# Performance work log

Measured on AMD Instinct MI355X. Metric: run time of the kernel, lower is better.

The kernel has to match this reference:

```python
import jax, jax.numpy as jnp
import numpy as np

EMBED_DIM = 1024
N_HEAD = 16
HEAD_DIM = EMBED_DIM // N_HEAD


def setup_inputs() -> dict:
    key = jax.random.key(0)
    k1, k2, k3 = jax.random.split(key, 3)
    B, S = 2, 2048
    x = jax.random.normal(k1, (B, S, EMBED_DIM), dtype=jnp.float32)
    # kaiming-style scale for the packed QKV projection and output projection
    w_qkv = jax.random.normal(k2, (3 * EMBED_DIM, EMBED_DIM), dtype=jnp.float32) * np.sqrt(2.0 / EMBED_DIM)
    w0 = jax.random.normal(k3, (EMBED_DIM, EMBED_DIM), dtype=jnp.float32) * np.sqrt(2.0 / EMBED_DIM)
    return {"x": x, "w_qkv": w_qkv, "w0": w0}


def reference(x, w_qkv, w0):
    B, S, E = x.shape
    # fused QKV projection (Linear with no bias): x @ w_qkv.T -> [B,S,3E]
    qkv = jnp.einsum('bse,fe->bsf', x, w_qkv)
    q, k, v = jnp.split(qkv, 3, axis=-1)
    # reshape to [B, H, S, D]
    def heads(t):
        return t.reshape(B, S, N_HEAD, HEAD_DIM).transpose(0, 2, 1, 3)
    q, k, v = heads(q), heads(k), heads(v)
    scale = 1.0 / np.sqrt(HEAD_DIM).astype(np.float32)
    scores = jnp.einsum('bhsd,bhtd->bhst', q, k) * scale  # [B,H,S,S]
    # causal additive bias: -inf above the diagonal (same math as the precomputed bias tensor)
    causal = jnp.tril(jnp.ones((S, S), dtype=bool))
    scores = jnp.where(causal, scores, -jnp.inf)
    probs = jax.nn.softmax(scores, axis=-1)
    e = jnp.einsum('bhst,bhtd->bhsd', probs, v)  # [B,H,S,D]
    e = e.transpose(0, 2, 1, 3).reshape(B, S, E)
    # output projection: E @ w0.T
    return jnp.einsum('bse,fe->bsf', e, w0)
```

## Files before the change

### kernel.cpp

```cpp
#include <hip/hip_runtime.h>


typedef unsigned short u16;
typedef short bf16x8 __attribute__((ext_vector_type(8)));
typedef float f32x4 __attribute__((ext_vector_type(4)));
typedef unsigned short u16x4 __attribute__((ext_vector_type(4)));

#define S_LEN 2048
#define EMB 1024
#define NH 16
#define HD 64
#define QKV_W 3072
#define BATCH 2
#define CSC 0.18033688f
#define PSTR 72

static __device__ __forceinline__ u16 f2bf(float f) {
    unsigned x = __float_as_uint(f);
    return (u16)((x + 0x7fffu + ((x >> 16) & 1u)) >> 16);
}

static __device__ __forceinline__ void gld_lds16(const u16* g, u16* l) {
    __builtin_amdgcn_global_load_lds(
        (const __attribute__((address_space(1))) void*)g,
        (__attribute__((address_space(3))) void*)l, 16, 0, 0);
}

#define XN4 (BATCH * S_LEN * EMB / 4)
#define WQ4 (QKV_W * EMB / 4)
#define W04 (EMB * EMB / 4)
__global__ __launch_bounds__(256) void cvt_all(const float* __restrict__ x,
                                               const float* __restrict__ wq,
                                               const float* __restrict__ w0,
                                               u16* __restrict__ xb,
                                               u16* __restrict__ wqb,
                                               u16* __restrict__ w0b) {
    int i = blockIdx.x * 256 + threadIdx.x;
    const float* src;
    u16* dst;
    int off;
    if (i < XN4) { src = x; dst = xb; off = i; }
    else if (i < XN4 + WQ4) { src = wq; dst = wqb; off = i - XN4; }
    else { src = w0; dst = w0b; off = i - XN4 - WQ4; }
    float4 v = ((const float4*)src)[off];
    u16x4 o;
    o[0] = f2bf(v.x); o[1] = f2bf(v.y); o[2] = f2bf(v.z); o[3] = f2bf(v.w);
    ((u16x4*)dst)[off] = o;
}

template <typename OutT, int BN>
__global__ __launch_bounds__(256) void gemm_bt(const u16* __restrict__ A,
                                               const u16* __restrict__ Bt,
                                               OutT* __restrict__ C,
                                               int M, int N, int K, int qcols) {
    constexpr int NF = BN / 32;
    __shared__ alignas(16) u16 As[128 * 32];
    __shared__ alignas(16) u16 Bs[BN * 32];
    const int tid = threadIdx.x;
    const int wave = tid >> 6, lane = tid & 63;
    const int quad = lane >> 4, lr = lane & 15;
    const int m0 = blockIdx.y * 128, n0 = blockIdx.x * BN;
    const int wm = (wave & 1) * 64, wn = (wave >> 1) * (BN / 2);
    const float sc = (n0 < qcols) ? CSC : 1.0f;

    f32x4 acc[4][NF] = {};

    for (int k0 = 0; k0 < K; k0 += 32) {
#pragma unroll
        for (int i = 0; i < 2; ++i) {
            int chunk = tid + i * 256;
            int row = chunk >> 2;
            int col8 = (chunk & 3) * 8;
            gld_lds16(&A[(size_t)(m0 + row) * K + k0 + col8], &As[row * 32 + col8]);
        }
#pragma unroll
        for (int i = 0; i < BN / 64; ++i) {
            int chunk = tid + i * 256;
            int row = chunk >> 2;
            int col8 = (chunk & 3) * 8;
            gld_lds16(&Bt[(size_t)(n0 + row) * K + k0 + col8], &Bs[row * 32 + col8]);
        }
        __syncthreads();
        bf16x8 af[4], bf[NF];
#pragma unroll
        for (int i = 0; i < 4; ++i)
            af[i] = *(const bf16x8*)&As[(wm + i * 16 + lr) * 32 + quad * 8];
#pragma unroll
        for (int i = 0; i < NF; ++i)
            bf[i] = *(const bf16x8*)&Bs[(wn + i * 16 + lr) * 32 + quad * 8];
#pragma unroll
        for (int mi = 0; mi < 4; ++mi)
#pragma unroll
            for (int ni = 0; ni < NF; ++ni)
                acc[mi][ni] = __builtin_amdgcn_mfma_f32_16x16x32_bf16(
                    af[mi], bf[ni], acc[mi][ni], 0, 0, 0);
        __syncthreads();
    }

#pragma unroll
    for (int mi = 0; mi < 4; ++mi) {
#pragma unroll
        for (int r = 0; r < 4; ++r) {
            int gr = m0 + wm + mi * 16 + quad * 4 + r;
#pragma unroll
            for (int ni = 0; ni < NF; ++ni) {
                int gc = n0 + wn + ni * 16 + lr;
                float v = acc[mi][ni][r] * sc;
                if constexpr (sizeof(OutT) == 2)
                    C[(size_t)gr * N + gc] = (OutT)f2bf(v);
                else
                    C[(size_t)gr * N + gc] = (OutT)v;
            }
        }
    }
}

__global__ __launch_bounds__(256) void transpose_v(const u16* __restrict__ qkv,
                                                   u16* __restrict__ vt) {
    __shared__ alignas(16) u16 t[64][72];
    const int s0 = blockIdx.x * 64;
    const int bh = blockIdx.y;
    const int b = bh >> 4, h = bh & 15;
#pragma unroll
    for (int i = 0; i < 2; ++i) {
        int chunk = threadIdx.x + i * 256;
        int row = chunk >> 3;
        int c8 = (chunk & 7) * 8;
        uint4 v = *(const uint4*)&qkv[(size_t)(b * S_LEN + s0 + row) * QKV_W +
                                      2 * EMB + h * HD + c8];
        const u16* p = (const u16*)&v;
#pragma unroll
        for (int jj = 0; jj < 8; ++jj) t[c8 + jj][row] = p[jj];
    }
    __syncthreads();
#pragma unroll
    for (int i = 0; i < 2; ++i) {
        int chunk = threadIdx.x + i * 256;
        int d = chunk >> 3;
        int c8 = (chunk & 7) * 8;
        uint4 v = *(const uint4*)&t[d][c8];
        *(uint4*)&vt[((size_t)bh * HD + d) * S_LEN + s0 + c8] = v;
    }
}

__global__ __launch_bounds__(512, 4) void attn(const u16* __restrict__ qkv,
                                               const u16* __restrict__ vt,
                                               u16* __restrict__ e) {
    const int tid = threadIdx.x;
    const int w = tid >> 6, lane = tid & 63;
    const int quad = lane >> 4, lr = lane & 15;
    const int pi = blockIdx.x;
    const int qtB = 31 - pi;
    const int bh = blockIdx.y, b = bh >> 4, h = bh & 15;
    const int myqt = (w < 4) ? pi : qtB;
    const int qbase = myqt * 64 + (w & 3) * 16;

    __shared__ alignas(16) u16 Ks[2 * 2 * 64 * 32];
    __shared__ alignas(16) u16 Vs[2 * 2 * 64 * 32];
    __shared__ alignas(16) u16 plds[8][16 * PSTR];
    u16* pw = plds[w];

    const u16* qkv_b = qkv + (size_t)b * S_LEN * QKV_W;
    const u16* qrow = qkv_b + (size_t)(qbase + lr) * QKV_W + h * HD + quad * 8;
    const bf16x8 qf0 = *(const bf16x8*)(qrow);
    const bf16x8 qf1 = *(const bf16x8*)(qrow + 32);

    const u16* kbase = qkv_b + EMB + h * HD;
    const u16* vbase = vt + (size_t)bh * HD * S_LEN;

    f32x4 o[4] = {};
    float lsum = 0.f;
    const int qg = qbase + lr;

    const int sr = (w & 3) * 16 + (lane >> 2);
    const int sc = (lane & 3) * 8;

    auto stage = [&](int j, int bb) {
        const int kv0 = j * 64;
        if (w < 4) {
            gld_lds16(kbase + (size_t)(kv0 + sr) * QKV_W + sc,
                      &Ks[bb * 4096 + sr * 32 + sc]);
            gld_lds16(kbase + (size_t)(kv0 + sr) * QKV_W + 32 + sc,
                      &Ks[bb * 4096 + 2048 + sr * 32 + sc]);
        } else {
            gld_lds16(vbase + (size_t)sr * S_LEN + kv0 + sc,
                      &Vs[bb * 4096 + sr * 32 + sc]);
            gld_lds16(vbase + (size_t)sr * S_LEN + kv0 + 32 + sc,
                      &Vs[bb * 4096 + 2048 + sr * 32 + sc]);
        }
    };

    stage(0, 0);
    for (int j = 0; j <= qtB; ++j) {
        const int bb = j & 1;
        __syncthreads();
        if (j < qtB) stage(j + 1, 1 - bb);
        if (j <= myqt) {
            const int kv0 = j * 64;
            const u16* ks = &Ks[bb * 4096];
            const u16* vs = &Vs[bb * 4096];
            f32x4 s[4];
#pragma unroll
            for (int nt = 0; nt < 4; ++nt) {
                bf16x8 k0 = *(const bf16x8*)&ks[(nt * 16 + lr) * 32 + quad * 8];
                bf16x8 k1 = *(const bf16x8*)&ks[2048 + (nt * 16 + lr) * 32 + quad * 8];
                f32x4 z = {};
                z = __builtin_amdgcn_mfma_f32_16x16x32_bf16(k0, qf0, z, 0, 0, 0);
                z = __builtin_amdgcn_mfma_f32_16x16x32_bf16(k1, qf1, z, 0, 0, 0);
                s[nt] = z;
            }
            const bool diag = (j == myqt);
            __builtin_amdgcn_wave_barrier();
#pragma unroll
            for (int nt = 0; nt < 4; ++nt) {
                float p[4];
#pragma unroll
                for (int r = 0; r < 4; ++r) {
                    float pv = exp2f(s[nt][r]);
                    if (diag) pv = (kv0 + nt * 16 + quad * 4 + r > qg) ? 0.f : pv;
                    p[r] = pv;
                }
                lsum += (p[0] + p[1]) + (p[2] + p[3]);
                uint2 pk;
                pk.x = __builtin_amdgcn_perm(__float_as_uint(p[1]),
                                             __float_as_uint(p[0]), 0x07060302u);
                pk.y = __builtin_amdgcn_perm(__float_as_uint(p[3]),
                                             __float_as_uint(p[2]), 0x07060302u);
                *(uint2*)&pw[lr * PSTR + nt * 16 + quad * 4] = pk;
            }
            __builtin_amdgcn_wave_barrier();
            const bf16x8 p0 = *(const bf16x8*)&pw[lr * PSTR + quad * 8];
            const bf16x8 p1 = *(const bf16x8*)&pw[lr * PSTR + 32 + quad * 8];
#pragma unroll
            for (int nt = 0; nt < 4; ++nt) {
                bf16x8 v0 = *(const bf16x8*)&vs[(nt * 16 + lr) * 32 + quad * 8];
                bf16x8 v1 = *(const bf16x8*)&vs[2048 + (nt * 16 + lr) * 32 + quad * 8];
                o[nt] = __builtin_amdgcn_mfma_f32_16x16x32_bf16(p0, v0, o[nt], 0, 0, 0);
                o[nt] = __builtin_amdgcn_mfma_f32_16x16x32_bf16(p1, v1, o[nt], 0, 0, 0);
            }
        }
    }

    float lf = lsum + __shfl_xor(lsum, 16, 64);
    lf += __shfl_xor(lf, 32, 64);
#pragma unroll
    for (int r = 0; r < 4; ++r) {
        float inv = 1.0f / __shfl(lf, quad * 4 + r, 64);
        size_t row = (size_t)(b * S_LEN + qbase + quad * 4 + r) * EMB + h * HD;
#pragma unroll
        for (int nt = 0; nt < 4; ++nt)
            e[row + nt * 16 + lr] = f2bf(o[nt][r] * inv);
    }
}

extern "C" void kernel_launch(void* const* d_in, const int* in_sizes, int n_in,
                              void* d_out, int out_size, void* d_ws, size_t ws_size,
                              hipStream_t stream) {
    const float* x = (const float*)d_in[0];
    const float* w_qkv = (const float*)d_in[1];
    const float* w0 = (const float*)d_in[2];
    float* out = (float*)d_out;

    const size_t M = (size_t)BATCH * S_LEN;
    u16* xb = (u16*)d_ws;
    u16* wqb = xb + M * EMB;
    u16* w0b = wqb + (size_t)QKV_W * EMB;
    u16* qkvb = w0b + (size_t)EMB * EMB;
    u16* vtb = qkvb + M * QKV_W;
    u16* eb = vtb + (size_t)BATCH * NH * HD * S_LEN;

    cvt_all<<<(XN4 + WQ4 + W04) / 256, 256, 0, stream>>>(x, w_qkv, w0, xb, wqb, w0b);

    gemm_bt<u16, 128><<<dim3(QKV_W / 128, M / 128), 256, 0, stream>>>(
        xb, wqb, qkvb, (int)M, QKV_W, EMB, EMB);

    transpose_v<<<dim3(S_LEN / 64, BATCH * NH), 256, 0, stream>>>(qkvb, vtb);

    attn<<<dim3(16, BATCH * NH), 512, 0, stream>>>(qkvb, vtb, eb);

    gemm_bt<float, 64><<<dim3(EMB / 64, M / 128), 256, 0, stream>>>(
        eb, w0b, out, (int)M, EMB, EMB, 0);
}
```

Measured before the change: 188.6 us.

## Split KV tile across wave halves so all waves process both paired query tiles

In the attention kernel, each block handles a pair of causal query tiles. Previously half the waves owned tile A and half owned tile B, so the A waves idled once their shorter causal range ended. Now every wave computes both tiles but only over half of each 64-wide KV block, and the two halves' partial outputs and row sums are merged through shared memory at the end. This balances MFMA work across all eight waves and reuses each K/V fragment for two queries. The cost is extra registers for two accumulator sets, which may hurt occupancy, plus an extra LDS reduction and synchronisation.

Measured after the change: 185.9 us. About the same (-1.4%).

```diff
diff --git a/kernel.cpp b/kernel.cpp
--- a/kernel.cpp
+++ b/kernel.cpp
@@ -149,30 +149,33 @@
     const int tid = threadIdx.x;
     const int w = tid >> 6, lane = tid & 63;
     const int quad = lane >> 4, lr = lane & 15;
-    const int pi = blockIdx.x;
-    const int qtB = 31 - pi;
+    const int wq = w & 3, hv = w >> 2;
+    const int tA = blockIdx.x;
+    const int tB = 31 - tA;
     const int bh = blockIdx.y, b = bh >> 4, h = bh & 15;
-    const int myqt = (w < 4) ? pi : qtB;
-    const int qbase = myqt * 64 + (w & 3) * 16;
-
-    __shared__ alignas(16) u16 Ks[2 * 2 * 64 * 32];
-    __shared__ alignas(16) u16 Vs[2 * 2 * 64 * 32];
-    __shared__ alignas(16) u16 plds[8][16 * PSTR];
-    u16* pw = plds[w];
+
+    __shared__ alignas(16) u16 smem[25600];
+    u16* Ks = smem;
+    u16* Vs = smem + 8192;
+    u16* pw = smem + 16384 + w * 16 * PSTR;
 
     const u16* qkv_b = qkv + (size_t)b * S_LEN * QKV_W;
-    const u16* qrow = qkv_b + (size_t)(qbase + lr) * QKV_W + h * HD + quad * 8;
-    const bf16x8 qf0 = *(const bf16x8*)(qrow);
-    const bf16x8 qf1 = *(const bf16x8*)(qrow + 32);
+    const u16* qrowA = qkv_b + (size_t)(tA * 64 + wq * 16 + lr) * QKV_W + h * HD + quad * 8;
+    const u16* qrowB = qkv_b + (size_t)(tB * 64 + wq * 16 + lr) * QKV_W + h * HD + quad * 8;
+    const bf16x8 qfA0 = *(const bf16x8*)(qrowA);
+    const bf16x8 qfA1 = *(const bf16x8*)(qrowA + 32);
+    const bf16x8 qfB0 = *(const bf16x8*)(qrowB);
+    const bf16x8 qfB1 = *(const bf16x8*)(qrowB + 32);
 
     const u16* kbase = qkv_b + EMB + h * HD;
     const u16* vbase = vt + (size_t)bh * HD * S_LEN;
 
-    f32x4 o[4] = {};
-    float lsum = 0.f;
-    const int qg = qbase + lr;
-
-    const int sr = (w & 3) * 16 + (lane >> 2);
+    f32x4 oA[4] = {}, oB[4] = {};
+    float lsA = 0.f, lsB = 0.f;
+    const int qgA = tA * 64 + wq * 16 + lr;
+    const int qgB = tB * 64 + wq * 16 + lr;
+
+    const int sr = wq * 16 + (lane >> 2);
     const int sc = (lane & 3) * 8;
 
     auto stage = [&](int j, int bb) {
@@ -191,65 +194,131 @@
     };
 
     stage(0, 0);
-    for (int j = 0; j <= qtB; ++j) {
+    for (int j = 0; j <= tB; ++j) {
         const int bb = j & 1;
         __syncthreads();
-        if (j < qtB) stage(j + 1, 1 - bb);
-        if (j <= myqt) {
-            const int kv0 = j * 64;
-            const u16* ks = &Ks[bb * 4096];
-            const u16* vs = &Vs[bb * 4096];
-            f32x4 s[4];
-#pragma unroll
-            for (int nt = 0; nt < 4; ++nt) {
-                bf16x8 k0 = *(const bf16x8*)&ks[(nt * 16 + lr) * 32 + quad * 8];
-                bf16x8 k1 = *(const bf16x8*)&ks[2048 + (nt * 16 + lr) * 32 + quad * 8];
-                f32x4 z = {};
-                z = __builtin_amdgcn_mfma_f32_16x16x32_bf16(k0, qf0, z, 0, 0, 0);
-                z = __builtin_amdgcn_mfma_f32_16x16x32_bf16(k1, qf1, z, 0, 0, 0);
-                s[nt] = z;
+        if (j < tB) stage(j + 1, 1 - bb);
+        const bool doA = (j <= tA);
+        const u16* ks = &Ks[bb * 4096];
+        const u16* vs = &Vs[bb * 4096];
+        const int kvh = hv * 32;
+
+        f32x4 sB[2], sA[2];
+#pragma unroll
+        for (int nt = 0; nt < 2; ++nt) {
+            const int kvr = kvh + nt * 16 + lr;
+            bf16x8 k0 = *(const bf16x8*)&ks[kvr * 32 + quad * 8];
+            bf16x8 k1 = *(const bf16x8*)&ks[2048 + kvr * 32 + quad * 8];
+            f32x4 z = {};
+            z = __builtin_amdgcn_mfma_f32_16x16x32_bf16(k0, qfB0, z, 0, 0, 0);
+            z = __builtin_amdgcn_mfma_f32_16x16x32_bf16(k1, qfB1, z, 0, 0, 0);
+            sB[nt] = z;
+            if (doA) {
+                f32x4 za = {};
+                za = __builtin_amdgcn_mfma_f32_16x16x32_bf16(k0, qfA0, za, 0, 0, 0);
+                za = __builtin_amdgcn_mfma_f32_16x16x32_bf16(k1, qfA1, za, 0, 0, 0);
+                sA[nt] = za;
             }
-            const bool diag = (j == myqt);
-            __builtin_amdgcn_wave_barrier();
-#pragma unroll
-            for (int nt = 0; nt < 4; ++nt) {
+        }
+
+        const int kvg = j * 64 + kvh;
+        __builtin_amdgcn_wave_barrier();
+#pragma unroll
+        for (int nt = 0; nt < 2; ++nt) {
+            float p[4];
+#pragma unroll
+            for (int r = 0; r < 4; ++r) {
+                float pv = exp2f(sB[nt][r]);
+                if (j == tB) pv = (kvg + nt * 16 + quad * 4 + r > qgB) ? 0.f : pv;
+                p[r] = pv;
+            }
+            lsB += (p[0] + p[1]) + (p[2] + p[3]);
+            uint2 pk;
+            pk.x = __builtin_amdgcn_perm(__float_as_uint(p[1]),
+                                         __float_as_uint(p[0]), 0x07060302u);
+            pk.y = __builtin_amdgcn_perm(__float_as_uint(p[3]),
+                                         __float_as_uint(p[2]), 0x07060302u);
+            *(uint2*)&pw[lr * PSTR + nt * 16 + quad * 4] = pk;
+        }
+        if (doA) {
+#pragma unroll
+            for (int nt = 0; nt < 2; ++nt) {
                 float p[4];
 #pragma unroll
                 for (int r = 0; r < 4; ++r) {
-                    float pv = exp2f(s[nt][r]);
-                    if (diag) pv = (kv0 + nt * 16 + quad * 4 + r > qg) ? 0.f : pv;
+                    float pv = exp2f(sA[nt][r]);
+                    if (j == tA) pv = (kvg + nt * 16 + quad * 4 + r > qgA) ? 0.f : pv;
                     p[r] = pv;
                 }
-                lsum += (p[0] + p[1]) + (p[2] + p[3]);
+                lsA += (p[0] + p[1]) + (p[2] + p[3]);
                 uint2 pk;
                 pk.x = __builtin_amdgcn_perm(__float_as_uint(p[1]),
                                              __float_as_uint(p[0]), 0x07060302u);
                 pk.y = __builtin_amdgcn_perm(__float_as_uint(p[3]),
                                              __float_as_uint(p[2]), 0x07060302u);
-                *(uint2*)&pw[lr * PSTR + nt * 16 + quad * 4] = pk;
+                *(uint2*)&pw[lr * PSTR + 32 + nt * 16 + quad * 4] = pk;
             }
-            __builtin_amdgcn_wave_barrier();
-            const bf16x8 p0 = *(const bf16x8*)&pw[lr * PSTR + quad * 8];
-            const bf16x8 p1 = *(const bf16x8*)&pw[lr * PSTR + 32 + quad * 8];
-#pragma unroll
-            for (int nt = 0; nt < 4; ++nt) {
-                bf16x8 v0 = *(const bf16x8*)&vs[(nt * 16 + lr) * 32 + quad * 8];
-                bf16x8 v1 = *(const bf16x8*)&vs[2048 + (nt * 16 + lr) * 32 + quad * 8];
-                o[nt] = __builtin_amdgcn_mfma_f32_16x16x32_bf16(p0, v0, o[nt], 0, 0, 0);
-                o[nt] = __builtin_amdgcn_mfma_f32_16x16x32_bf16(p1, v1, o[nt], 0, 0, 0);
-            }
-        }
-    }
-
-    float lf = lsum + __shfl_xor(lsum, 16, 64);
-    lf += __shfl_xor(lf, 32, 64);
-#pragma unroll
-    for (int r = 0; r < 4; ++r) {
-        float inv = 1.0f / __shfl(lf, quad * 4 + r, 64);
-        size_t row = (size_t)(b * S_LEN + qbase + quad * 4 + r) * EMB + h * HD;
+        }
+        __builtin_amdgcn_wave_barrier();
+        const bf16x8 pB = *(const bf16x8*)&pw[lr * PSTR + quad * 8];
+        bf16x8 pA = {};
+        if (doA) pA = *(const bf16x8*)&pw[lr * PSTR + 32 + quad * 8];
+
+#pragma unroll
+        for (int nt = 0; nt < 4; ++nt) {
+            bf16x8 v = *(const bf16x8*)&vs[hv * 2048 + (nt * 16 + lr) * 32 + quad * 8];
+            oB[nt] = __builtin_amdgcn_mfma_f32_16x16x32_bf16(pB, v, oB[nt], 0, 0, 0);
+            if (doA) oA[nt] = __builtin_amdgcn_mfma_f32_16x16x32_bf16(pA, v, oA[nt], 0, 0, 0);
+        }
+    }
+
+    float lfA = lsA + __shfl_xor(lsA, 16, 64);
+    lfA += __shfl_xor(lfA, 32, 64);
+    float lfB = lsB + __shfl_xor(lsB, 16, 64);
+    lfB += __shfl_xor(lfB, 32, 64);
+    __syncthreads();
+    float* mA = (float*)smem;
+    float* mB = mA + 64 * 66;
+    float* lAr = mB + 64 * 66;
+    float* lBr = lAr + 64;
+    if (hv) {
 #pragma unroll
         for (int nt = 0; nt < 4; ++nt)
-            e[row + nt * 16 + lr] = f2bf(o[nt][r] * inv);
+#pragma unroll
+            for (int r = 0; r < 4; ++r)
+                mA[(wq * 16 + quad * 4 + r) * 66 + nt * 16 + lr] = oA[nt][r];
+        if (lane < 16) lAr[wq * 16 + lane] = lfA;
+    } else {
+#pragma unroll
+        for (int nt = 0; nt < 4; ++nt)
+#pragma unroll
+            for (int r = 0; r < 4; ++r)
+                mB[(wq * 16 + quad * 4 + r) * 66 + nt * 16 + lr] = oB[nt][r];
+        if (lane < 16) lBr[wq * 16 + lane] = lfB;
+    }
+    __syncthreads();
+    if (!hv) {
+        float lff = lfA + lAr[wq * 16 + lr];
+#pragma unroll
+        for (int r = 0; r < 4; ++r) {
+            float inv = 1.0f / __shfl(lff, quad * 4 + r, 64);
+            size_t row = (size_t)(b * S_LEN + tA * 64 + wq * 16 + quad * 4 + r) * EMB + h * HD;
+#pragma unroll
+            for (int nt = 0; nt < 4; ++nt)
+                e[row + nt * 16 + lr] =
+                    f2bf((oA[nt][r] + mA[(wq * 16 + quad * 4 + r) * 66 + nt * 16 + lr]) * inv);
+        }
+    } else {
+        float lff = lfB + lBr[wq * 16 + lr];
+#pragma unroll
+        for (int r = 0; r < 4; ++r) {
+            float inv = 1.0f / __shfl(lff, quad * 4 + r, 64);
+            size_t row = (size_t)(b * S_LEN + tB * 64 + wq * 16 + quad * 4 + r) * EMB + h * HD;
+#pragma unroll
+            for (int nt = 0; nt < 4; ++nt)
+                e[row + nt * 16 + lr] =
+                    f2bf((oB[nt][r] + mB[(wq * 16 + quad * 4 + r) * 66 + nt * 16 + lr]) * inv);
+        }
     }
 }
 
```
